# Kernel optimization log

Hardware: AMD Instinct MI355X
Metric: run time of the kernel (lower is better)

## Reference

```python
import jax, jax.numpy as jnp
import numpy as np

BITS = 4
GROUPSIZE = 128
IN_FEATURES = 4096
OUT_FEATURES = 4096
GROUPS = IN_FEATURES // GROUPSIZE  # 32
TOKENS = 8192


def setup_inputs() -> dict:
    key = jax.random.key(0)
    k_x, k_s, k_b = jax.random.split(key, 3)
    rng = np.random.default_rng(0)
    # packed 4-bit weights: 8 nibbles per int32 word
    qweight = jnp.asarray(
        rng.integers(-2**31, 2**31, size=(IN_FEATURES // 8, OUT_FEATURES), dtype=np.int64).astype(np.int32)
    )
    qzeros = jnp.asarray(
        rng.integers(-2**31, 2**31, size=(GROUPS, OUT_FEATURES // 8), dtype=np.int64).astype(np.int32)
    )
    scales = jax.random.uniform(k_s, (GROUPS, OUT_FEATURES), dtype=jnp.float32) * 0.02 + 0.001
    g_idx = (jnp.arange(IN_FEATURES, dtype=jnp.int32) // GROUPSIZE).astype(jnp.int32)
    bias = jax.random.normal(k_b, (OUT_FEATURES,), dtype=jnp.float32) * 0.01
    x = jax.random.normal(k_x, (TOKENS, IN_FEATURES), dtype=jnp.float32)
    return {"x": x, "qweight": qweight, "qzeros": qzeros, "scales": scales,
            "g_idx": g_idx, "bias": bias}


def reference(x, qweight, qzeros, scales, g_idx, bias):
    out_features = qweight.shape[1]
    in_features = qweight.shape[0] * 8
    mask = jnp.int32(15)  # 2**bits - 1
    wf = jnp.arange(0, 32, BITS, dtype=jnp.int32)  # [8] nibble shift amounts
    # unpack zero points: [groups, out//8, 8] -> [groups, out]
    zeros = ((qzeros[:, :, None] >> wf[None, None, :]) & mask) + 1
    zeros = zeros.reshape(scales.shape)
    # unpack weights: [in//8, 8, out] -> [in, out]
    weight = (qweight[:, None, :] >> wf[None, :, None]) & mask
    weight = weight.reshape(in_features, out_features)
    # dequantize per group and matmul
    W = scales[g_idx] * (weight - zeros[g_idx]).astype(scales.dtype)
    out = x @ W
    return out + bias
```

## Files before the change

### kernel.cpp

```cpp
#include <hip/hip_runtime.h>
#include <cstdint>
#include <cstddef>

#define IN_F   4096
#define OUT_F  4096
#define NTOK   8192
#define NGRP   32

#define BM 256
#define BN 256
#define BK 64
#define KTILES   (IN_F / BK)
#define LDS_TILE (BM * BK)

typedef __attribute__((ext_vector_type(8))) __bf16 bf16x8;
typedef __attribute__((ext_vector_type(4))) float  floatx4;

__device__ __forceinline__ unsigned short f2bf(float f) {
    unsigned int u = __builtin_bit_cast(unsigned int, f);
    u += 0x7fffu + ((u >> 16) & 1u);
    return (unsigned short)(u >> 16);
}

__device__ __forceinline__ void gload16(const void* g, void* l) {
    __builtin_amdgcn_global_load_lds(
        (const __attribute__((address_space(1))) void*)g,
        (__attribute__((address_space(3))) void*)l,
        16, 0, 0);
}

__global__ void dequant_kernel(const int* __restrict__ qweight,
                               const int* __restrict__ qzeros,
                               const float* __restrict__ scales,
                               const int* __restrict__ g_idx,
                               unsigned short* __restrict__ Wt) {
    __shared__ unsigned short tile[256 * 64];
    const int tk  = blockIdx.x & 63;
    const int tn  = blockIdx.x >> 6;
    const int tid = threadIdx.x;
    const int n   = tn * 256 + tid;

#pragma unroll
    for (int r = 0; r < 8; ++r) {
        const int k8 = tk * 8 + r;
        const int k  = k8 * 8;
        const int g  = g_idx[k];
        const int qw = qweight[(size_t)k8 * OUT_F + n];
        const float s = scales[g * OUT_F + n];
        const int  zw = qzeros[g * (OUT_F / 8) + (n >> 3)];
        const float z = (float)(((zw >> (4 * (n & 7))) & 15) + 1);
        const float sz = s * z;
        union { unsigned short h[8]; uint4 v; } u;
#pragma unroll
        for (int j = 0; j < 8; ++j)
            u.h[j] = f2bf(s * (float)((qw >> (4 * j)) & 15) - sz);
        *(uint4*)(tile + tid * 64 + ((r ^ (tid & 7)) * 8)) = u.v;
    }
    __syncthreads();
#pragma unroll
    for (int i = 0; i < 8; ++i) {
        const int nl = i * 32 + (tid >> 3);
        const int c  = tid & 7;
        const uint4 v = *(const uint4*)(tile + nl * 64 + ((c ^ (nl & 7)) * 8));
        *(uint4*)(Wt + (size_t)(tn * 256 + nl) * IN_F + tk * 64 + c * 8) = v;
    }
}

__global__ void xcast_kernel(const float* __restrict__ x,
                             unsigned short* __restrict__ Xb) {
    const size_t i = ((size_t)blockIdx.x * 256 + threadIdx.x) * 8;
    const float4 a = *(const float4*)(x + i);
    const float4 b = *(const float4*)(x + i + 4);
    union { unsigned short h[8]; uint4 v; } u;
    u.h[0] = f2bf(a.x); u.h[1] = f2bf(a.y); u.h[2] = f2bf(a.z); u.h[3] = f2bf(a.w);
    u.h[4] = f2bf(b.x); u.h[5] = f2bf(b.y); u.h[6] = f2bf(b.z); u.h[7] = f2bf(b.w);
    *(uint4*)(Xb + i) = u.v;
}

#define VMCNT0() asm volatile("s_waitcnt vmcnt(0)" ::: "memory")
#define BAR() do { asm volatile("" ::: "memory"); \
                   __builtin_amdgcn_s_barrier();  \
                   asm volatile("" ::: "memory"); } while (0)

template<int I0, int J0>
__device__ __forceinline__ void quad(floatx4 (&acc)[8][4],
                                     const bf16x8 (&av)[4][2],
                                     const bf16x8 (&bv)[4][2]) {
#pragma unroll
    for (int i4 = 0; i4 < 4; ++i4)
#pragma unroll
        for (int jj = 0; jj < 2; ++jj)
#pragma unroll
            for (int kk = 0; kk < 2; ++kk)
                acc[I0 + i4][J0 + jj] = __builtin_amdgcn_mfma_f32_16x16x32_bf16(
                    av[i4][kk], bv[J0 + jj][kk], acc[I0 + i4][J0 + jj], 0, 0, 0);
}

__global__ __launch_bounds__(512, 2) void gemm_kernel(
        const unsigned short* __restrict__ Xb,
        const unsigned short* __restrict__ Wt,
        const float* __restrict__ bias,
        float* __restrict__ out) {
    __shared__ unsigned short As[2 * LDS_TILE];
    __shared__ unsigned short Bs[2 * LDS_TILE];

    const int tid  = threadIdx.x;
    const int wave = tid >> 6;
    const int lane = tid & 63;
    const int mi   = lane & 15;
    const int kq   = lane >> 4;

    const int bid = blockIdx.x;
    const int swz = (bid & 7) * 64 + (bid >> 3);
    const int m0  = (swz >> 4) * BM;
    const int n0  = (swz & 15) * BN;

    const int wrow = (wave >> 2) * 128;
    const int wcol = (wave & 3) * 64;

    const int lrow   = lane >> 3;
    const int lchunk = ((lane & 7) ^ lrow) * 8;
    const unsigned short* aSrc = Xb + (size_t)(m0 + lrow) * IN_F + lchunk;
    const unsigned short* bSrc = Wt + (size_t)(n0 + lrow) * IN_F + lchunk;

    const int raA = (wave >> 2) * 128 + (wave & 3) * 16;
    const int raB = (wave >> 1) * 64  + (wave & 1) * 16;

    const int aRd = (wrow + mi) * BK;
    const int bRd = (wcol + mi) * BK;
    const int cp0 = ((kq)     ^ (mi & 7)) * 8;
    const int cp1 = ((4 + kq) ^ (mi & 7)) * 8;

    floatx4 acc[8][4];
#pragma unroll
    for (int i = 0; i < 8; ++i)
#pragma unroll
        for (int j = 0; j < 4; ++j)
            acc[i][j] = floatx4{0.f, 0.f, 0.f, 0.f};

    bf16x8 av[4][2], bv[4][2];

    auto stageA = [&](int bufofs, int h, int kt) {
        const int r0 = raA + h * 64;
        gload16(aSrc + (size_t)(r0 + 0) * IN_F + (size_t)kt * BK,
                (void*)(As + bufofs + (r0 + 0) * BK));
        gload16(aSrc + (size_t)(r0 + 8) * IN_F + (size_t)kt * BK,
                (void*)(As + bufofs + (r0 + 8) * BK));
    };
    auto stageB = [&](int bufofs, int h, int kt) {
        const int r0 = raB + h * 32;
        gload16(bSrc + (size_t)(r0 + 0) * IN_F + (size_t)kt * BK,
                (void*)(Bs + bufofs + (r0 + 0) * BK));
        gload16(bSrc + (size_t)(r0 + 8) * IN_F + (size_t)kt * BK,
                (void*)(Bs + bufofs + (r0 + 8) * BK));
    };
    auto stageAll = [&](int bufofs, int kt) {
        stageA(bufofs, 0, kt);
        stageB(bufofs, 0, kt);
        stageB(bufofs, 1, kt);
        stageA(bufofs, 1, kt);
    };
    auto ldah = [&](int bufofs, int ah) {
#pragma unroll
        for (int i4 = 0; i4 < 4; ++i4) {
            av[i4][0] = *(const bf16x8*)(As + bufofs + aRd + (ah * 4 + i4) * (16 * BK) + cp0);
            av[i4][1] = *(const bf16x8*)(As + bufofs + aRd + (ah * 4 + i4) * (16 * BK) + cp1);
        }
    };
    auto ldb01 = [&](int bufofs) {
#pragma unroll
        for (int jj = 0; jj < 2; ++jj) {
            bv[jj][0] = *(const bf16x8*)(Bs + bufofs + bRd + jj * (16 * BK) + cp0);
            bv[jj][1] = *(const bf16x8*)(Bs + bufofs + bRd + jj * (16 * BK) + cp1);
        }
    };
    auto ldb23 = [&](int bufofs) {
#pragma unroll
        for (int jj = 0; jj < 2; ++jj) {
            bv[2 + jj][0] = *(const bf16x8*)(Bs + bufofs + bRd + (2 + jj) * (16 * BK) + cp0);
            bv[2 + jj][1] = *(const bf16x8*)(Bs + bufofs + bRd + (2 + jj) * (16 * BK) + cp1);
        }
    };

    stageAll(0, 0);
    VMCNT0();
    BAR();

    for (int kt = 0; kt < KTILES; ++kt) {
        const int bo = (kt & 1) * LDS_TILE;
        const int no = bo ^ LDS_TILE;

        if (kt < KTILES - 1)
            stageAll(no, kt + 1);

        ldah(bo, 0); ldb01(bo);
        quad<0, 0>(acc, av, bv);
        ldb23(bo);
        quad<0, 2>(acc, av, bv);
        ldah(bo, 1);
        quad<4, 2>(acc, av, bv);
        quad<4, 0>(acc, av, bv);

        if (kt < KTILES - 1) {
            VMCNT0();
            BAR();
        }
    }

    const int mq = kq;
#pragma unroll
    for (int j = 0; j < 4; ++j) {
        const int col = n0 + wcol + j * 16 + mi;
        const float bb = bias[col];
#pragma unroll
        for (int i = 0; i < 8; ++i) {
#pragma unroll
            for (int r = 0; r < 4; ++r) {
                const int row = m0 + wrow + i * 16 + mq * 4 + r;
                out[(size_t)row * OUT_F + col] = acc[i][j][r] + bb;
            }
        }
    }
}

extern "C" void kernel_launch(void* const* d_in, const int* in_sizes, int n_in,
                              void* d_out, int out_size, void* d_ws, size_t ws_size,
                              hipStream_t stream) {
    const float* x       = (const float*)d_in[0];
    const int*   qweight = (const int*)d_in[1];
    const int*   qzeros  = (const int*)d_in[2];
    const float* scales  = (const float*)d_in[3];
    const int*   g_idx   = (const int*)d_in[4];
    const float* bias    = (const float*)d_in[5];
    float*       out     = (float*)d_out;

    unsigned short* Wt = (unsigned short*)d_ws;
    unsigned short* Xb = Wt + (size_t)OUT_F * IN_F;

    dequant_kernel<<<64 * 16, 256, 0, stream>>>(qweight, qzeros, scales, g_idx, Wt);
    xcast_kernel<<<((size_t)NTOK * IN_F / 8) / 256, 256, 0, stream>>>(x, Xb);

    gemm_kernel<<<dim3((NTOK / BM) * (OUT_F / BN)), 512, 0, stream>>>(Xb, Wt, bias, out);
}
```

Before: 539.6 us.

## Double GEMM waves per block and fuse weight dequant with activation cast

Splits the 256x256 GEMM tile across 16 waves (each 64x64) instead of 8 waves (each 128x64), halving per-wave accumulators and spreading global-to-LDS staging across all waves. The aim is more latency hiding through more resident waves. The trade-off is lower per-wave register reuse and higher LDS read traffic per MFMA. The dequantization and fp32-to-bf16 activation cast are also merged into one launch to remove a kernel launch.

After: 513.8 us. 1.05x faster.

```diff
diff --git a/kernel.cpp b/kernel.cpp
--- a/kernel.cpp
+++ b/kernel.cpp
@@ -29,52 +29,54 @@
         16, 0, 0);
 }
 
-__global__ void dequant_kernel(const int* __restrict__ qweight,
-                               const int* __restrict__ qzeros,
-                               const float* __restrict__ scales,
-                               const int* __restrict__ g_idx,
-                               unsigned short* __restrict__ Wt) {
+__global__ void prep_kernel(const int* __restrict__ qweight,
+                            const int* __restrict__ qzeros,
+                            const float* __restrict__ scales,
+                            const int* __restrict__ g_idx,
+                            const float* __restrict__ x,
+                            unsigned short* __restrict__ Wt,
+                            unsigned short* __restrict__ Xb) {
     __shared__ unsigned short tile[256 * 64];
-    const int tk  = blockIdx.x & 63;
-    const int tn  = blockIdx.x >> 6;
     const int tid = threadIdx.x;
-    const int n   = tn * 256 + tid;
-
-#pragma unroll
-    for (int r = 0; r < 8; ++r) {
-        const int k8 = tk * 8 + r;
-        const int k  = k8 * 8;
-        const int g  = g_idx[k];
-        const int qw = qweight[(size_t)k8 * OUT_F + n];
-        const float s = scales[g * OUT_F + n];
-        const int  zw = qzeros[g * (OUT_F / 8) + (n >> 3)];
-        const float z = (float)(((zw >> (4 * (n & 7))) & 15) + 1);
-        const float sz = s * z;
+
+    if (blockIdx.x < 1024) {
+        const int tk  = blockIdx.x & 63;
+        const int tn  = blockIdx.x >> 6;
+        const int n   = tn * 256 + tid;
+
+#pragma unroll
+        for (int r = 0; r < 8; ++r) {
+            const int k8 = tk * 8 + r;
+            const int k  = k8 * 8;
+            const int g  = g_idx[k];
+            const int qw = qweight[(size_t)k8 * OUT_F + n];
+            const float s = scales[g * OUT_F + n];
+            const int  zw = qzeros[g * (OUT_F / 8) + (n >> 3)];
+            const float z = (float)(((zw >> (4 * (n & 7))) & 15) + 1);
+            const float sz = s * z;
+            union { unsigned short h[8]; uint4 v; } u;
+#pragma unroll
+            for (int j = 0; j < 8; ++j)
+                u.h[j] = f2bf(s * (float)((qw >> (4 * j)) & 15) - sz);
+            *(uint4*)(tile + tid * 64 + ((r ^ (tid & 7)) * 8)) = u.v;
+        }
+        __syncthreads();
+#pragma unroll
+        for (int i = 0; i < 8; ++i) {
+            const int nl = i * 32 + (tid >> 3);
+            const int c  = tid & 7;
+            const uint4 v = *(const uint4*)(tile + nl * 64 + ((c ^ (nl & 7)) * 8));
+            *(uint4*)(Wt + (size_t)(tn * 256 + nl) * IN_F + tk * 64 + c * 8) = v;
+        }
+    } else {
+        const size_t i = ((size_t)(blockIdx.x - 1024) * 256 + tid) * 8;
+        const float4 a = *(const float4*)(x + i);
+        const float4 b = *(const float4*)(x + i + 4);
         union { unsigned short h[8]; uint4 v; } u;
-#pragma unroll
-        for (int j = 0; j < 8; ++j)
-            u.h[j] = f2bf(s * (float)((qw >> (4 * j)) & 15) - sz);
-        *(uint4*)(tile + tid * 64 + ((r ^ (tid & 7)) * 8)) = u.v;
+        u.h[0] = f2bf(a.x); u.h[1] = f2bf(a.y); u.h[2] = f2bf(a.z); u.h[3] = f2bf(a.w);
+        u.h[4] = f2bf(b.x); u.h[5] = f2bf(b.y); u.h[6] = f2bf(b.z); u.h[7] = f2bf(b.w);
+        *(uint4*)(Xb + i) = u.v;
     }
-    __syncthreads();
-#pragma unroll
-    for (int i = 0; i < 8; ++i) {
-        const int nl = i * 32 + (tid >> 3);
-        const int c  = tid & 7;
-        const uint4 v = *(const uint4*)(tile + nl * 64 + ((c ^ (nl & 7)) * 8));
-        *(uint4*)(Wt + (size_t)(tn * 256 + nl) * IN_F + tk * 64 + c * 8) = v;
-    }
-}
-
-__global__ void xcast_kernel(const float* __restrict__ x,
-                             unsigned short* __restrict__ Xb) {
-    const size_t i = ((size_t)blockIdx.x * 256 + threadIdx.x) * 8;
-    const float4 a = *(const float4*)(x + i);
-    const float4 b = *(const float4*)(x + i + 4);
-    union { unsigned short h[8]; uint4 v; } u;
-    u.h[0] = f2bf(a.x); u.h[1] = f2bf(a.y); u.h[2] = f2bf(a.z); u.h[3] = f2bf(a.w);
-    u.h[4] = f2bf(b.x); u.h[5] = f2bf(b.y); u.h[6] = f2bf(b.z); u.h[7] = f2bf(b.w);
-    *(uint4*)(Xb + i) = u.v;
 }
 
 #define VMCNT0() asm volatile("s_waitcnt vmcnt(0)" ::: "memory")
@@ -82,8 +84,8 @@
                    __builtin_amdgcn_s_barrier();  \
                    asm volatile("" ::: "memory"); } while (0)
 
-template<int I0, int J0>
-__device__ __forceinline__ void quad(floatx4 (&acc)[8][4],
+template<int J0>
+__device__ __forceinline__ void quad(floatx4 (&acc)[4][4],
                                      const bf16x8 (&av)[4][2],
                                      const bf16x8 (&bv)[4][2]) {
 #pragma unroll
@@ -92,11 +94,11 @@
         for (int jj = 0; jj < 2; ++jj)
 #pragma unroll
             for (int kk = 0; kk < 2; ++kk)
-                acc[I0 + i4][J0 + jj] = __builtin_amdgcn_mfma_f32_16x16x32_bf16(
-                    av[i4][kk], bv[J0 + jj][kk], acc[I0 + i4][J0 + jj], 0, 0, 0);
-}
-
-__global__ __launch_bounds__(512, 2) void gemm_kernel(
+                acc[i4][J0 + jj] = __builtin_amdgcn_mfma_f32_16x16x32_bf16(
+                    av[i4][kk], bv[J0 + jj][kk], acc[i4][J0 + jj], 0, 0, 0);
+}
+
+__global__ __launch_bounds__(1024) void gemm_kernel(
         const unsigned short* __restrict__ Xb,
         const unsigned short* __restrict__ Wt,
         const float* __restrict__ bias,
@@ -115,7 +117,7 @@
     const int m0  = (swz >> 4) * BM;
     const int n0  = (swz & 15) * BN;
 
-    const int wrow = (wave >> 2) * 128;
+    const int wrow = (wave >> 2) * 64;
     const int wcol = (wave & 3) * 64;
 
     const int lrow   = lane >> 3;
@@ -123,48 +125,37 @@
     const unsigned short* aSrc = Xb + (size_t)(m0 + lrow) * IN_F + lchunk;
     const unsigned short* bSrc = Wt + (size_t)(n0 + lrow) * IN_F + lchunk;
 
-    const int raA = (wave >> 2) * 128 + (wave & 3) * 16;
-    const int raB = (wave >> 1) * 64  + (wave & 1) * 16;
+    const int ra = wave * 16;
 
     const int aRd = (wrow + mi) * BK;
     const int bRd = (wcol + mi) * BK;
     const int cp0 = ((kq)     ^ (mi & 7)) * 8;
     const int cp1 = ((4 + kq) ^ (mi & 7)) * 8;
 
-    floatx4 acc[8][4];
-#pragma unroll
-    for (int i = 0; i < 8; ++i)
+    floatx4 acc[4][4];
+#pragma unroll
+    for (int i = 0; i < 4; ++i)
 #pragma unroll
         for (int j = 0; j < 4; ++j)
             acc[i][j] = floatx4{0.f, 0.f, 0.f, 0.f};
 
     bf16x8 av[4][2], bv[4][2];
 
-    auto stageA = [&](int bufofs, int h, int kt) {
-        const int r0 = raA + h * 64;
-        gload16(aSrc + (size_t)(r0 + 0) * IN_F + (size_t)kt * BK,
-                (void*)(As + bufofs + (r0 + 0) * BK));
-        gload16(aSrc + (size_t)(r0 + 8) * IN_F + (size_t)kt * BK,
-                (void*)(As + bufofs + (r0 + 8) * BK));
-    };
-    auto stageB = [&](int bufofs, int h, int kt) {
-        const int r0 = raB + h * 32;
-        gload16(bSrc + (size_t)(r0 + 0) * IN_F + (size_t)kt * BK,
-                (void*)(Bs + bufofs + (r0 + 0) * BK));
-        gload16(bSrc + (size_t)(r0 + 8) * IN_F + (size_t)kt * BK,
-                (void*)(Bs + bufofs + (r0 + 8) * BK));
-    };
     auto stageAll = [&](int bufofs, int kt) {
-        stageA(bufofs, 0, kt);
-        stageB(bufofs, 0, kt);
-        stageB(bufofs, 1, kt);
-        stageA(bufofs, 1, kt);
-    };
-    auto ldah = [&](int bufofs, int ah) {
+        gload16(aSrc + (size_t)(ra + 0) * IN_F + (size_t)kt * BK,
+                (void*)(As + bufofs + (ra + 0) * BK));
+        gload16(aSrc + (size_t)(ra + 8) * IN_F + (size_t)kt * BK,
+                (void*)(As + bufofs + (ra + 8) * BK));
+        gload16(bSrc + (size_t)(ra + 0) * IN_F + (size_t)kt * BK,
+                (void*)(Bs + bufofs + (ra + 0) * BK));
+        gload16(bSrc + (size_t)(ra + 8) * IN_F + (size_t)kt * BK,
+                (void*)(Bs + bufofs + (ra + 8) * BK));
+    };
+    auto lda = [&](int bufofs) {
 #pragma unroll
         for (int i4 = 0; i4 < 4; ++i4) {
-            av[i4][0] = *(const bf16x8*)(As + bufofs + aRd + (ah * 4 + i4) * (16 * BK) + cp0);
-            av[i4][1] = *(const bf16x8*)(As + bufofs + aRd + (ah * 4 + i4) * (16 * BK) + cp1);
+            av[i4][0] = *(const bf16x8*)(As + bufofs + aRd + i4 * (16 * BK) + cp0);
+            av[i4][1] = *(const bf16x8*)(As + bufofs + aRd + i4 * (16 * BK) + cp1);
         }
     };
     auto ldb01 = [&](int bufofs) {
@@ -193,13 +184,10 @@
         if (kt < KTILES - 1)
             stageAll(no, kt + 1);
 
-        ldah(bo, 0); ldb01(bo);
-        quad<0, 0>(acc, av, bv);
+        lda(bo); ldb01(bo);
+        quad<0>(acc, av, bv);
         ldb23(bo);
-        quad<0, 2>(acc, av, bv);
-        ldah(bo, 1);
-        quad<4, 2>(acc, av, bv);
-        quad<4, 0>(acc, av, bv);
+        quad<2>(acc, av, bv);
 
         if (kt < KTILES - 1) {
             VMCNT0();
@@ -213,7 +201,7 @@
         const int col = n0 + wcol + j * 16 + mi;
         const float bb = bias[col];
 #pragma unroll
-        for (int i = 0; i < 8; ++i) {
+        for (int i = 0; i < 4; ++i) {
 #pragma unroll
             for (int r = 0; r < 4; ++r) {
                 const int row = m0 + wrow + i * 16 + mq * 4 + r;
@@ -237,8 +225,8 @@
     unsigned short* Wt = (unsigned short*)d_ws;
     unsigned short* Xb = Wt + (size_t)OUT_F * IN_F;
 
-    dequant_kernel<<<64 * 16, 256, 0, stream>>>(qweight, qzeros, scales, g_idx, Wt);
-    xcast_kernel<<<((size_t)NTOK * IN_F / 8) / 256, 256, 0, stream>>>(x, Xb);
-
-    gemm_kernel<<<dim3((NTOK / BM) * (OUT_F / BN)), 512, 0, stream>>>(Xb, Wt, bias, out);
-}
+    prep_kernel<<<1024 + 16384, 256, 0, stream>>>(qweight, qzeros, scales,
+                                                  g_idx, x, Wt, Xb);
+
+    gemm_kernel<<<dim3((NTOK / BM) * (OUT_F / BN)), 1024, 0, stream>>>(Xb, Wt, bias, out);
+}
```
